# Kernel tuning notes

Hardware: AMD Instinct MI355X
Metric: run time of the kernel (lower is better)

Reference implementation:

```python
import jax, jax.numpy as jnp
import numpy as np

B, S, D, E = 4, 4096, 1024, 8

def setup_inputs() -> dict:
    key = jax.random.key(0)
    k_h, k_wr, k_br, k_we = jax.random.split(key, 4)
    h = jax.random.normal(k_h, (B, S, D), dtype=jnp.float32)
    # route_weights: nn.Linear(D, E) -> weight [E, D], bias [E]
    W_route = jax.random.normal(k_wr, (E, D), dtype=jnp.float32) / np.sqrt(D)
    b_route = jax.random.normal(k_br, (E,), dtype=jnp.float32) * 0.01
    # edge_transforms: E x nn.Linear(D, D, bias=False) -> stacked [E, D_out, D_in]
    W_edges = jax.random.normal(k_we, (E, D, D), dtype=jnp.float32) / np.sqrt(D)
    layer_bias = jnp.zeros((D,), dtype=jnp.float32)
    return {"h": h, "W_route": W_route, "b_route": b_route,
            "W_edges": W_edges, "layer_bias": layer_bias}

def reference(h, W_route, b_route, W_edges, layer_bias):
    # route_logits = h @ W_route.T + b_route -> [B, S, E]
    route_logits = jnp.einsum('bsd,ed->bse', h, W_route) + b_route
    rw = jax.nn.softmax(route_logits, axis=-1)
    # fused: sum_e rw[b,s,e] * (h @ W_e.T) -> [B, S, D]
    out = jnp.einsum('bsd,efd,bse->bsf', h, W_edges, rw)
    out = out + layer_bias
    return jax.nn.gelu(out, approximate=False)  # torch F.gelu default is exact erf
```

## Files before the change

kernel.cpp:

```cpp
#include <hip/hip_runtime.h>
#include <hip/hip_bf16.h>

#define M_TOK 16384
#define DDIM  1024
#define NEXP  8
#define KP    (NEXP * DDIM)

typedef __bf16 bf16x8 __attribute__((ext_vector_type(8)));
typedef float  floatx4 __attribute__((ext_vector_type(4)));

__device__ __forceinline__ void gload_lds16(const void* g, void* l) {
    __builtin_amdgcn_global_load_lds(
        (__attribute__((address_space(1))) void*)(void*)g,
        (__attribute__((address_space(3))) void*)l,
        16, 0, 0);
}

__global__ __launch_bounds__(256) void route_kernel(
    const float* __restrict__ h, const float* __restrict__ Wr,
    const float* __restrict__ br, __bf16* __restrict__ hbf,
    float* __restrict__ rw)
{
    __shared__ float Wrs[NEXP * DDIM];
    const int tid = threadIdx.x;
    {
        const float4* s4 = (const float4*)Wr;
        float4* d4 = (float4*)Wrs;
        #pragma unroll
        for (int j = 0; j < 8; ++j) d4[j * 256 + tid] = s4[j * 256 + tid];
    }
    __syncthreads();

    const int wave = tid >> 6, lane = tid & 63;
    const int m = blockIdx.x * 4 + wave;

    const float4* hrow = (const float4*)(h + (size_t)m * DDIM + lane * 16);
    float a[16];
    #pragma unroll
    for (int i = 0; i < 4; ++i) {
        float4 v = hrow[i];
        a[i*4+0] = v.x; a[i*4+1] = v.y; a[i*4+2] = v.z; a[i*4+3] = v.w;
    }
    bf16x8 o0, o1;
    #pragma unroll
    for (int i = 0; i < 8; ++i) { o0[i] = (__bf16)a[i]; o1[i] = (__bf16)a[8 + i]; }
    *(bf16x8*)(hbf + (size_t)m * DDIM + lane * 16)     = o0;
    *(bf16x8*)(hbf + (size_t)m * DDIM + lane * 16 + 8) = o1;

    float p[NEXP];
    #pragma unroll
    for (int e = 0; e < NEXP; ++e) {
        const float4* w4 = (const float4*)&Wrs[e * DDIM + lane * 16];
        float s = 0.f;
        #pragma unroll
        for (int i = 0; i < 4; ++i) {
            float4 wv = w4[i];
            s += a[i*4+0]*wv.x + a[i*4+1]*wv.y + a[i*4+2]*wv.z + a[i*4+3]*wv.w;
        }
        p[e] = s;
    }
    #pragma unroll
    for (int e = 0; e < NEXP; ++e) {
        #pragma unroll
        for (int off = 32; off > 0; off >>= 1)
            p[e] += __shfl_xor(p[e], off, 64);
    }
    if (lane == 0) {
        float l[NEXP], mx = -1e30f;
        #pragma unroll
        for (int e = 0; e < NEXP; ++e) { l[e] = p[e] + br[e]; mx = fmaxf(mx, l[e]); }
        float s = 0.f;
        #pragma unroll
        for (int e = 0; e < NEXP; ++e) { l[e] = expf(l[e] - mx); s += l[e]; }
        float inv = 1.f / s;
        float4 r0 = {l[0]*inv, l[1]*inv, l[2]*inv, l[3]*inv};
        float4 r1 = {l[4]*inv, l[5]*inv, l[6]*inv, l[7]*inv};
        *(float4*)(rw + (size_t)m * NEXP)     = r0;
        *(float4*)(rw + (size_t)m * NEXP + 4) = r1;
    }
}

__global__ __launch_bounds__(256) void convw2_kernel(
    const float* __restrict__ src, __bf16* __restrict__ dst)
{
    size_t idx = ((size_t)blockIdx.x * 256 + threadIdx.x) * 16;
    int e = (int)(idx >> 20);
    int f = (int)(idx >> 10) & 1023;
    int k = (int)idx & 1023;
    const float4* s4 = (const float4*)(src + idx);
    float a[16];
    #pragma unroll
    for (int i = 0; i < 4; ++i) {
        float4 v = s4[i];
        a[i*4+0] = v.x; a[i*4+1] = v.y; a[i*4+2] = v.z; a[i*4+3] = v.w;
    }
    bf16x8 o0, o1;
    #pragma unroll
    for (int i = 0; i < 8; ++i) { o0[i] = (__bf16)a[i]; o1[i] = (__bf16)a[8 + i]; }
    __bf16* d = dst + (size_t)f * KP + (size_t)e * DDIM + k;
    *(bf16x8*)d       = o0;
    *(bf16x8*)(d + 8) = o1;
}

__global__ __launch_bounds__(256, 3) void gemm_fused_kernel(
    const __bf16* __restrict__ hbf, const __bf16* __restrict__ Bp,
    const float* __restrict__ rw, const float* __restrict__ bias,
    float* __restrict__ outp)
{
    __shared__ __bf16 As[128 * 64];
    __shared__ __bf16 Bs[128 * 64];
    __shared__ float  rws[128 * NEXP];

    const int tid  = threadIdx.x;
    const int wave = tid >> 6, lane = tid & 63;
    const int quad = lane >> 4, l16 = lane & 15;
    const int wm = wave & 1, wn = wave >> 1;
    const int m0 = blockIdx.y * 128, f0 = blockIdx.x * 128;

    {
        const float4* src = (const float4*)(rw + (size_t)m0 * NEXP);
        ((float4*)rws)[tid] = src[tid];
    }

    const floatx4 z4 = {0.f, 0.f, 0.f, 0.f};
    floatx4 facc[4][4];
    #pragma unroll
    for (int i = 0; i < 4; ++i) {
        #pragma unroll
        for (int j = 0; j < 4; ++j) facc[i][j] = z4;
    }

    int aslot[2][4], bslot[2][4];
    #pragma unroll
    for (int s = 0; s < 2; ++s) {
        #pragma unroll
        for (int f = 0; f < 4; ++f) {
            int ra = wm*64 + f*16 + l16;
            int rb = wn*64 + f*16 + l16;
            int grp = s*4 + quad;
            aslot[s][f] = ra*8 + ((grp ^ ra) & 7);
            bslot[s][f] = rb*8 + ((grp ^ rb) & 7);
        }
    }

    __syncthreads();

    float wcur[4][4];

    for (int e = 0; e < NEXP; ++e) {
        #pragma unroll
        for (int mf = 0; mf < 4; ++mf) {
            #pragma unroll
            for (int r = 0; r < 4; ++r) {
                float wn_ = fmaxf(rws[(wm*64 + mf*16 + quad*4 + r) * NEXP + e], 1e-20f);
                if (e > 0) {
                    float ratio = wcur[mf][r] / wn_;
                    #pragma unroll
                    for (int nf = 0; nf < 4; ++nf)
                        facc[mf][nf][r] *= ratio;
                }
                wcur[mf][r] = wn_;
            }
        }

        for (int k0 = 0; k0 < DDIM; k0 += 64) {
            __syncthreads();
            #pragma unroll
            for (int t = 0; t < 4; ++t) {
                int g   = t * 256 + tid;
                int row = g >> 3;
                int c   = ((g ^ row) & 7) * 8;
                gload_lds16(hbf + (size_t)(m0 + row) * DDIM + k0 + c,
                            (char*)As + g * 16);
                gload_lds16(Bp + (size_t)(f0 + row) * KP + e * DDIM + k0 + c,
                            (char*)Bs + g * 16);
            }
            __syncthreads();

            #pragma unroll
            for (int s = 0; s < 2; ++s) {
                bf16x8 av[4], bv[4];
                #pragma unroll
                for (int mf = 0; mf < 4; ++mf)
                    av[mf] = *(const bf16x8*)&As[aslot[s][mf] * 8];
                #pragma unroll
                for (int nf = 0; nf < 4; ++nf)
                    bv[nf] = *(const bf16x8*)&Bs[bslot[s][nf] * 8];
                #pragma unroll
                for (int mf = 0; mf < 4; ++mf) {
                    #pragma unroll
                    for (int nf = 0; nf < 4; ++nf)
                        facc[mf][nf] = __builtin_amdgcn_mfma_f32_16x16x32_bf16(
                            av[mf], bv[nf], facc[mf][nf], 0, 0, 0);
                }
            }
        }
    }

    #pragma unroll
    for (int nf = 0; nf < 4; ++nf) {
        int gf = f0 + wn*64 + nf*16 + l16;
        float bval = bias[gf];
        #pragma unroll
        for (int mf = 0; mf < 4; ++mf) {
            int gm = m0 + wm*64 + mf*16 + quad*4;
            #pragma unroll
            for (int r = 0; r < 4; ++r) {
                float x = facc[mf][nf][r] * wcur[mf][r] + bval;
                float gel = 0.5f * x * (1.0f + erff(x * 0.70710678118f));
                outp[(size_t)(gm + r) * DDIM + gf] = gel;
            }
        }
    }
}

extern "C" void kernel_launch(void* const* d_in, const int* in_sizes, int n_in,
                              void* d_out, int out_size, void* d_ws, size_t ws_size,
                              hipStream_t stream) {
    const float* h    = (const float*)d_in[0];
    const float* Wr   = (const float*)d_in[1];
    const float* br   = (const float*)d_in[2];
    const float* We   = (const float*)d_in[3];
    const float* bias = (const float*)d_in[4];
    float* outp = (float*)d_out;
    char* ws = (char*)d_ws;

    __bf16* hbf = (__bf16*)ws;
    __bf16* Bp  = (__bf16*)(ws + (size_t)M_TOK * DDIM * 2);
    float*  rwp = (float*)(ws + (size_t)M_TOK * DDIM * 2
                              + (size_t)NEXP * DDIM * DDIM * 2);

    hipLaunchKernelGGL(route_kernel, dim3(M_TOK / 4), dim3(256), 0, stream,
                       h, Wr, br, hbf, rwp);
    hipLaunchKernelGGL(convw2_kernel, dim3((NEXP * DDIM * DDIM) / (256 * 16)),
                       dim3(256), 0, stream, We, Bp);
    hipLaunchKernelGGL(gemm_fused_kernel, dim3(DDIM / 128, M_TOK / 128),
                       dim3(256), 0, stream, hbf, Bp, rwp, bias, outp);
}
```

Baseline: 505.8 us.

## Merge prep kernels and rebuild GEMM with 256x256 tiles and 4-stage pipeline

```diff
diff --git a/kernel.cpp b/kernel.cpp
--- a/kernel.cpp
+++ b/kernel.cpp
@@ -7,6 +7,7 @@
 #define KP    (NEXP * DDIM)
 
 typedef __bf16 bf16x8 __attribute__((ext_vector_type(8)));
+typedef __bf16 bf16x4 __attribute__((ext_vector_type(4)));
 typedef float  floatx4 __attribute__((ext_vector_type(4)));
 
 __device__ __forceinline__ void gload_lds16(const void* g, void* l) {
@@ -16,13 +17,38 @@
         16, 0, 0);
 }
 
-__global__ __launch_bounds__(256) void route_kernel(
+#define CONV_BLOCKS  2048
+#define ROUTE_BLOCKS 4096
+
+__global__ __launch_bounds__(256) void prep_kernel(
     const float* __restrict__ h, const float* __restrict__ Wr,
-    const float* __restrict__ br, __bf16* __restrict__ hbf,
-    float* __restrict__ rw)
+    const float* __restrict__ br, const float* __restrict__ We,
+    __bf16* __restrict__ hbf, float* __restrict__ rw, __bf16* __restrict__ Bp)
 {
     __shared__ float Wrs[NEXP * DDIM];
     const int tid = threadIdx.x;
+
+    if (blockIdx.x < CONV_BLOCKS) {
+        size_t idx = ((size_t)blockIdx.x * 256 + tid) * 16;
+        int e = (int)(idx >> 20);
+        int f = (int)(idx >> 10) & 1023;
+        int k = (int)idx & 1023;
+        const float4* s4 = (const float4*)(We + idx);
+        float a[16];
+        #pragma unroll
+        for (int i = 0; i < 4; ++i) {
+            float4 v = s4[i];
+            a[i*4+0] = v.x; a[i*4+1] = v.y; a[i*4+2] = v.z; a[i*4+3] = v.w;
+        }
+        bf16x8 o0, o1;
+        #pragma unroll
+        for (int i = 0; i < 8; ++i) { o0[i] = (__bf16)a[i]; o1[i] = (__bf16)a[8 + i]; }
+        __bf16* d = Bp + (size_t)f * KP + (size_t)e * DDIM + k;
+        *(bf16x8*)d       = o0;
+        *(bf16x8*)(d + 8) = o1;
+        return;
+    }
+
     {
         const float4* s4 = (const float4*)Wr;
         float4* d4 = (float4*)Wrs;
@@ -32,30 +58,30 @@
     __syncthreads();
 
     const int wave = tid >> 6, lane = tid & 63;
-    const int m = blockIdx.x * 4 + wave;
-
-    const float4* hrow = (const float4*)(h + (size_t)m * DDIM + lane * 16);
-    float a[16];
-    #pragma unroll
-    for (int i = 0; i < 4; ++i) {
-        float4 v = hrow[i];
-        a[i*4+0] = v.x; a[i*4+1] = v.y; a[i*4+2] = v.z; a[i*4+3] = v.w;
-    }
-    bf16x8 o0, o1;
-    #pragma unroll
-    for (int i = 0; i < 8; ++i) { o0[i] = (__bf16)a[i]; o1[i] = (__bf16)a[8 + i]; }
-    *(bf16x8*)(hbf + (size_t)m * DDIM + lane * 16)     = o0;
-    *(bf16x8*)(hbf + (size_t)m * DDIM + lane * 16 + 8) = o1;
-
+    const int m = (blockIdx.x - CONV_BLOCKS) * 4 + wave;
+
+    const float4* hrow4 = (const float4*)(h + (size_t)m * DDIM);
+    float4 a[4];
+    #pragma unroll
+    for (int j = 0; j < 4; ++j) a[j] = hrow4[j * 64 + lane];
+
+    #pragma unroll
+    for (int j = 0; j < 4; ++j) {
+        bf16x4 o;
+        o[0] = (__bf16)a[j].x; o[1] = (__bf16)a[j].y;
+        o[2] = (__bf16)a[j].z; o[3] = (__bf16)a[j].w;
+        *(bf16x4*)(hbf + (size_t)m * DDIM + j * 256 + lane * 4) = o;
+    }
+
+    const float4* Wrs4 = (const float4*)Wrs;
     float p[NEXP];
     #pragma unroll
     for (int e = 0; e < NEXP; ++e) {
-        const float4* w4 = (const float4*)&Wrs[e * DDIM + lane * 16];
         float s = 0.f;
         #pragma unroll
-        for (int i = 0; i < 4; ++i) {
-            float4 wv = w4[i];
-            s += a[i*4+0]*wv.x + a[i*4+1]*wv.y + a[i*4+2]*wv.z + a[i*4+3]*wv.w;
+        for (int j = 0; j < 4; ++j) {
+            float4 wv = Wrs4[e * 256 + j * 64 + lane];
+            s += a[j].x*wv.x + a[j].y*wv.y + a[j].z*wv.z + a[j].w*wv.w;
         }
         p[e] = s;
     }
@@ -80,135 +106,145 @@
     }
 }
 
-__global__ __launch_bounds__(256) void convw2_kernel(
-    const float* __restrict__ src, __bf16* __restrict__ dst)
-{
-    size_t idx = ((size_t)blockIdx.x * 256 + threadIdx.x) * 16;
-    int e = (int)(idx >> 20);
-    int f = (int)(idx >> 10) & 1023;
-    int k = (int)idx & 1023;
-    const float4* s4 = (const float4*)(src + idx);
-    float a[16];
-    #pragma unroll
-    for (int i = 0; i < 4; ++i) {
-        float4 v = s4[i];
-        a[i*4+0] = v.x; a[i*4+1] = v.y; a[i*4+2] = v.z; a[i*4+3] = v.w;
-    }
-    bf16x8 o0, o1;
-    #pragma unroll
-    for (int i = 0; i < 8; ++i) { o0[i] = (__bf16)a[i]; o1[i] = (__bf16)a[8 + i]; }
-    __bf16* d = dst + (size_t)f * KP + (size_t)e * DDIM + k;
-    *(bf16x8*)d       = o0;
-    *(bf16x8*)(d + 8) = o1;
-}
-
-__global__ __launch_bounds__(256, 3) void gemm_fused_kernel(
+__global__ __launch_bounds__(512, 2) void gemm_fused_kernel(
     const __bf16* __restrict__ hbf, const __bf16* __restrict__ Bp,
     const float* __restrict__ rw, const float* __restrict__ bias,
     float* __restrict__ outp)
 {
-    __shared__ __bf16 As[128 * 64];
-    __shared__ __bf16 Bs[128 * 64];
-    __shared__ float  rws[128 * NEXP];
+    __shared__ __bf16 As[4][256 * 32];
+    __shared__ __bf16 Bs[4][256 * 32];
 
     const int tid  = threadIdx.x;
     const int wave = tid >> 6, lane = tid & 63;
     const int quad = lane >> 4, l16 = lane & 15;
-    const int wm = wave & 1, wn = wave >> 1;
-    const int m0 = blockIdx.y * 128, f0 = blockIdx.x * 128;
+    const int wm = wave >> 2, wn = wave & 3;
+    const int m0 = blockIdx.y * 256, f0 = blockIdx.x * 256;
+
+    const int arow = wm * 128 + l16;
+    const int brow = wn * 64  + l16;
+    const int aoff0 = (arow * 4 + (quad ^ ((arow >> 1) & 3))) * 16;
+    const int boff0 = (brow * 4 + (quad ^ ((brow >> 1) & 3))) * 16;
+
+    const int srow = tid >> 2;
+    const int scol = ((tid & 3) ^ ((srow >> 1) & 3)) * 8;
+    const int aBase = (m0 + srow) * DDIM + scol;
+    const int bBase = (f0 + srow) * KP + scol;
+
+    floatx4 facc[8][4];
+    const floatx4 z4 = {0.f, 0.f, 0.f, 0.f};
+    #pragma unroll
+    for (int i = 0; i < 8; ++i)
+        #pragma unroll
+        for (int j = 0; j < 4; ++j) facc[i][j] = z4;
 
     {
-        const float4* src = (const float4*)(rw + (size_t)m0 * NEXP);
-        ((float4*)rws)[tid] = src[tid];
-    }
-
-    const floatx4 z4 = {0.f, 0.f, 0.f, 0.f};
-    floatx4 facc[4][4];
-    #pragma unroll
-    for (int i = 0; i < 4; ++i) {
-        #pragma unroll
-        for (int j = 0; j < 4; ++j) facc[i][j] = z4;
-    }
-
-    int aslot[2][4], bslot[2][4];
-    #pragma unroll
-    for (int s = 0; s < 2; ++s) {
-        #pragma unroll
-        for (int f = 0; f < 4; ++f) {
-            int ra = wm*64 + f*16 + l16;
-            int rb = wn*64 + f*16 + l16;
-            int grp = s*4 + quad;
-            aslot[s][f] = ra*8 + ((grp ^ ra) & 7);
-            bslot[s][f] = rb*8 + ((grp ^ rb) & 7);
-        }
-    }
-
-    __syncthreads();
-
-    float wcur[4][4];
-
+        const __bf16* a0 = hbf + aBase;
+        const __bf16* b0 = Bp  + bBase;
+        gload_lds16(a0,                 (char*)&As[0][0] + tid * 16);
+        gload_lds16(b0,                 (char*)&Bs[0][0] + tid * 16);
+        gload_lds16(a0 + 131072,        (char*)&As[0][0] + tid * 16 + 8192);
+        gload_lds16(b0 + 1048576,       (char*)&Bs[0][0] + tid * 16 + 8192);
+        gload_lds16(a0 + 32,            (char*)&As[1][0] + tid * 16);
+        gload_lds16(b0 + 32,            (char*)&Bs[1][0] + tid * 16);
+        gload_lds16(a0 + 131072 + 32,   (char*)&As[1][0] + tid * 16 + 8192);
+        gload_lds16(b0 + 1048576 + 32,  (char*)&Bs[1][0] + tid * 16 + 8192);
+    }
+
+    #pragma unroll 1
     for (int e = 0; e < NEXP; ++e) {
-        #pragma unroll
-        for (int mf = 0; mf < 4; ++mf) {
+        if (e > 0) {
             #pragma unroll
-            for (int r = 0; r < 4; ++r) {
-                float wn_ = fmaxf(rws[(wm*64 + mf*16 + quad*4 + r) * NEXP + e], 1e-20f);
-                if (e > 0) {
-                    float ratio = wcur[mf][r] / wn_;
+            for (int mf = 0; mf < 8; ++mf) {
+                #pragma unroll
+                for (int r = 0; r < 4; ++r) {
+                    int row = m0 + wm * 128 + mf * 16 + quad * 4 + r;
+                    float wp = fmaxf(rw[(size_t)row * NEXP + e - 1], 1e-20f);
+                    float wc = fmaxf(rw[(size_t)row * NEXP + e],     1e-20f);
+                    float ratio = wp / wc;
                     #pragma unroll
-                    for (int nf = 0; nf < 4; ++nf)
-                        facc[mf][nf][r] *= ratio;
+                    for (int nf = 0; nf < 4; ++nf) facc[mf][nf][r] *= ratio;
                 }
-                wcur[mf][r] = wn_;
             }
         }
-
-        for (int k0 = 0; k0 < DDIM; k0 += 64) {
-            __syncthreads();
+        #pragma unroll 1
+        for (int kt4 = 0; kt4 < 8; ++kt4) {
             #pragma unroll
-            for (int t = 0; t < 4; ++t) {
-                int g   = t * 256 + tid;
-                int row = g >> 3;
-                int c   = ((g ^ row) & 7) * 8;
-                gload_lds16(hbf + (size_t)(m0 + row) * DDIM + k0 + c,
-                            (char*)As + g * 16);
-                gload_lds16(Bp + (size_t)(f0 + row) * KP + e * DDIM + k0 + c,
-                            (char*)Bs + g * 16);
-            }
-            __syncthreads();
-
-            #pragma unroll
-            for (int s = 0; s < 2; ++s) {
-                bf16x8 av[4], bv[4];
-                #pragma unroll
-                for (int mf = 0; mf < 4; ++mf)
-                    av[mf] = *(const bf16x8*)&As[aslot[s][mf] * 8];
+            for (int u = 0; u < 4; ++u) {
+                const int t  = (e << 5) + (kt4 << 2) + u;
+                const int tt = (t + 2) & 255;
+                const __bf16* asrc = hbf + aBase + ((tt & 31) << 5);
+                const __bf16* bsrc = Bp  + bBase + (tt << 5);
+                char* ad = (char*)&As[(u + 2) & 3][0] + tid * 16;
+                char* bd = (char*)&Bs[(u + 2) & 3][0] + tid * 16;
+                const char* Ab = (const char*)&As[u][0];
+                const char* Bb = (const char*)&Bs[u][0];
+
+                asm volatile("s_waitcnt vmcnt(4)" ::: "memory");
+                asm volatile("s_barrier" ::: "memory");
+
+                bf16x8 av0[4], bv[4];
+                #pragma unroll
+                for (int mf = 0; mf < 4; ++mf)
+                    av0[mf] = *(const bf16x8*)(Ab + aoff0 + mf * 1024);
                 #pragma unroll
                 for (int nf = 0; nf < 4; ++nf)
-                    bv[nf] = *(const bf16x8*)&Bs[bslot[s][nf] * 8];
-                #pragma unroll
-                for (int mf = 0; mf < 4; ++mf) {
+                    bv[nf] = *(const bf16x8*)(Bb + boff0 + nf * 1024);
+                gload_lds16(asrc, ad);
+                gload_lds16(bsrc, bd);
+
+                asm volatile("s_barrier" ::: "memory");
+                asm volatile("s_waitcnt lgkmcnt(0)" ::: "memory");
+                __builtin_amdgcn_sched_barrier(0);
+                __builtin_amdgcn_s_setprio(1);
+                #pragma unroll
+                for (int mf = 0; mf < 4; ++mf)
                     #pragma unroll
                     for (int nf = 0; nf < 4; ++nf)
                         facc[mf][nf] = __builtin_amdgcn_mfma_f32_16x16x32_bf16(
-                            av[mf], bv[nf], facc[mf][nf], 0, 0, 0);
-                }
+                            av0[mf], bv[nf], facc[mf][nf], 0, 0, 0);
+                __builtin_amdgcn_sched_barrier(0);
+                __builtin_amdgcn_s_setprio(0);
+                asm volatile("s_barrier" ::: "memory");
+
+                bf16x8 av1[4];
+                #pragma unroll
+                for (int mf = 0; mf < 4; ++mf)
+                    av1[mf] = *(const bf16x8*)(Ab + aoff0 + (4 + mf) * 1024);
+                gload_lds16(asrc + 131072,  ad + 8192);
+                gload_lds16(bsrc + 1048576, bd + 8192);
+
+                asm volatile("s_barrier" ::: "memory");
+                asm volatile("s_waitcnt lgkmcnt(0)" ::: "memory");
+                __builtin_amdgcn_sched_barrier(0);
+                __builtin_amdgcn_s_setprio(1);
+                #pragma unroll
+                for (int mf = 0; mf < 4; ++mf)
+                    #pragma unroll
+                    for (int nf = 0; nf < 4; ++nf)
+                        facc[4 + mf][nf] = __builtin_amdgcn_mfma_f32_16x16x32_bf16(
+                            av1[mf], bv[nf], facc[4 + mf][nf], 0, 0, 0);
+                __builtin_amdgcn_sched_barrier(0);
+                __builtin_amdgcn_s_setprio(0);
             }
         }
     }
 
-    #pragma unroll
-    for (int nf = 0; nf < 4; ++nf) {
-        int gf = f0 + wn*64 + nf*16 + l16;
-        float bval = bias[gf];
-        #pragma unroll
-        for (int mf = 0; mf < 4; ++mf) {
-            int gm = m0 + wm*64 + mf*16 + quad*4;
+    asm volatile("s_waitcnt vmcnt(0)" ::: "memory");
+
+    float bval[4];
+    #pragma unroll
+    for (int nf = 0; nf < 4; ++nf) bval[nf] = bias[f0 + wn * 64 + nf * 16 + l16];
+    #pragma unroll
+    for (int mf = 0; mf < 8; ++mf) {
+        #pragma unroll
+        for (int r = 0; r < 4; ++r) {
+            int gm = m0 + wm * 128 + mf * 16 + quad * 4 + r;
+            float w7 = fmaxf(rw[(size_t)gm * NEXP + 7], 1e-20f);
             #pragma unroll
-            for (int r = 0; r < 4; ++r) {
-                float x = facc[mf][nf][r] * wcur[mf][r] + bval;
+            for (int nf = 0; nf < 4; ++nf) {
+                float x = facc[mf][nf][r] * w7 + bval[nf];
                 float gel = 0.5f * x * (1.0f + erff(x * 0.70710678118f));
-                outp[(size_t)(gm + r) * DDIM + gf] = gel;
+                outp[(size_t)gm * DDIM + (f0 + wn * 64 + nf * 16 + l16)] = gel;
             }
         }
     }
@@ -230,10 +266,8 @@
     float*  rwp = (float*)(ws + (size_t)M_TOK * DDIM * 2
                               + (size_t)NEXP * DDIM * DDIM * 2);
 
-    hipLaunchKernelGGL(route_kernel, dim3(M_TOK / 4), dim3(256), 0, stream,
-                       h, Wr, br, hbf, rwp);
-    hipLaunchKernelGGL(convw2_kernel, dim3((NEXP * DDIM * DDIM) / (256 * 16)),
-                       dim3(256), 0, stream, We, Bp);
-    hipLaunchKernelGGL(gemm_fused_kernel, dim3(DDIM / 128, M_TOK / 128),
-                       dim3(256), 0, stream, hbf, Bp, rwp, bias, outp);
-}
+    hipLaunchKernelGGL(prep_kernel, dim3(CONV_BLOCKS + ROUTE_BLOCKS), dim3(256),
+                       0, stream, h, Wr, br, We, hbf, rwp, Bp);
+    hipLaunchKernelGGL(gemm_fused_kernel, dim3(DDIM / 256, M_TOK / 256),
+                       dim3(512), 0, stream, hbf, Bp, rwp, bias, outp);
+}
```

Measured after the change: 437.4 us. 1.16x faster.
